# Performance work log

Measured on AMD Instinct MI355X. Metric: run time of the kernel, lower is better.

## Reference

```python
import jax, jax.numpy as jnp
from jax import lax
import numpy as np

B = 128          # batch (matches module BATCH_SIZE)
H = W = 64       # image size
E = 8            # num_experts
K = 2            # top_k
C = 1000         # num_classes (expert hidden_size)
D = 14 * 14 * 64 # flattened conv features: 64->62->31->29->14


def setup_inputs() -> dict:
    key = jax.random.key(0)
    ks = jax.random.split(key, 10)
    return {
        "x": jax.random.normal(ks[0], (B, H, W, 1), dtype=jnp.float32),
        "conv1_w": jax.random.normal(ks[1], (3, 3, 1, 32), dtype=jnp.float32) * 0.05,
        "conv1_b": jnp.zeros((32,), dtype=jnp.float32),
        "conv2_w": jax.random.normal(ks[2], (3, 3, 32, 64), dtype=jnp.float32) * 0.05,
        "conv2_b": jnp.zeros((64,), dtype=jnp.float32),
        "gate_w": jax.random.normal(ks[3], (D, E), dtype=jnp.float32) * 0.001,
        "gate_b": jnp.zeros((E,), dtype=jnp.float32),
        "expert_w": jax.random.normal(ks[4], (E, D, C), dtype=jnp.float32) * 0.001,
        "expert_b": jnp.zeros((E, C), dtype=jnp.float32),
    }


def _conv_relu(x, w, b):
    y = lax.conv_general_dilated(x, w, window_strides=(1, 1), padding="VALID",
                                 dimension_numbers=("NHWC", "HWIO", "NHWC"))
    return jax.nn.relu(y + b)


def _maxpool2(x):
    return lax.reduce_window(x, -jnp.inf, lax.max,
                             (1, 2, 2, 1), (1, 2, 2, 1), "VALID")


def reference(x, conv1_w, conv1_b, conv2_w, conv2_b, gate_w, gate_b, expert_w, expert_b):
    # conv block (dropout is identity at inference)
    h = _maxpool2(_conv_relu(x, conv1_w, conv1_b))
    h = _maxpool2(_conv_relu(h, conv2_w, conv2_b))
    h = h.reshape(h.shape[0], -1)                       # [B, D]

    # gating: softmax + top-k
    gates = jax.nn.softmax(h @ gate_w + gate_b)         # [B, E]
    topk_w, topk_i = lax.top_k(gates, K)                # [B, K]

    # all experts (tiny dense layers stacked), then gather top-k and combine
    expert_out = jnp.einsum("bd,edc->bec", h, expert_w) + expert_b  # [B, E, C]
    sel = jnp.take_along_axis(expert_out, topk_i[:, :, None], axis=1)  # [B, K, C]
    combined = jnp.sum(sel * topk_w[:, :, None], axis=1)              # [B, C]

    return jax.nn.softmax(combined)
```

## Files before the change

### kernel.cpp

```cpp
#include <hip/hip_runtime.h>
#include <math.h>

#define D_FEAT 12544
#define NC 1000
#define RB 16
#define S4 32
#define DSLICE 392
#define NIT (DSLICE/4)
#define CT2 500

__global__ __launch_bounds__(256) void k1_conv1(
    const float* __restrict__ x, const float* __restrict__ w,
    const float* __restrict__ bias, float* __restrict__ h1)
{
    int co  = threadIdx.x & 31;
    int pxi = threadIdx.x >> 5;
    int blk = blockIdx.x;
    int pxg = blk & 3;
    int py  = (blk >> 2) % 31;
    int b   = blk / (31 * 4);
    int px  = pxg * 8 + pxi;
    if (px >= 31) return;

    float wr[9];
#pragma unroll
    for (int t = 0; t < 9; ++t) wr[t] = w[t * 32 + co];
    float bb = bias[co];

    float in[4][4];
    const float* xb = x + ((size_t)(b * 64 + 2 * py) * 64 + 2 * px);
#pragma unroll
    for (int r = 0; r < 4; ++r)
#pragma unroll
        for (int c = 0; c < 4; ++c)
            in[r][c] = xb[r * 64 + c];

    float a00 = 0.f, a01 = 0.f, a10 = 0.f, a11 = 0.f;
#pragma unroll
    for (int ky = 0; ky < 3; ++ky)
#pragma unroll
        for (int kx = 0; kx < 3; ++kx) {
            float wv = wr[ky * 3 + kx];
            a00 = fmaf(in[ky][kx],     wv, a00);
            a01 = fmaf(in[ky][kx + 1], wv, a01);
            a10 = fmaf(in[ky + 1][kx], wv, a10);
            a11 = fmaf(in[ky + 1][kx + 1], wv, a11);
        }
    a00 = fmaxf(a00 + bb, 0.f);
    a01 = fmaxf(a01 + bb, 0.f);
    a10 = fmaxf(a10 + bb, 0.f);
    a11 = fmaxf(a11 + bb, 0.f);
    float v = fmaxf(fmaxf(a00, a01), fmaxf(a10, a11));
    h1[((size_t)(b * 31 + py) * 31 + px) * 32 + co] = v;
}

__global__ __launch_bounds__(448) void k2_conv2(
    const float* __restrict__ h1, const float* __restrict__ w2,
    const float* __restrict__ b2, float* __restrict__ h)
{
    __shared__ float wl[9 * 32 * 32];

    int co  = threadIdx.x & 31;
    int px  = threadIdx.x >> 5;
    int blk = blockIdx.x;
    int cob = blk & 1;
    int py  = (blk >> 1) % 14;
    int b   = blk / 28;

    for (int i = threadIdx.x; i < 9 * 32 * 32; i += 448) {
        int tapci = i >> 5;
        int col   = i & 31;
        wl[i] = w2[tapci * 64 + cob * 32 + col];
    }
    __syncthreads();

    float acc00 = 0.f, acc01 = 0.f, acc10 = 0.f, acc11 = 0.f;
    const float* base = h1 + ((size_t)(b * 31 + 2 * py) * 31 + 2 * px) * 32;

    for (int q = 0; q < 8; ++q) {
        float4 in4[4][4];
#pragma unroll
        for (int r = 0; r < 4; ++r)
#pragma unroll
            for (int c = 0; c < 4; ++c)
                in4[r][c] = *(const float4*)(base + (r * 31 + c) * 32 + q * 4);

#pragma unroll
        for (int ky = 0; ky < 3; ++ky)
#pragma unroll
            for (int kx = 0; kx < 3; ++kx) {
                int tap = ky * 3 + kx;
                const float* wp = &wl[(tap * 32 + q * 4) * 32 + co];
                float w0 = wp[0];
                float w1 = wp[32];
                float w2v = wp[64];
                float w3 = wp[96];
                acc00 = fmaf(in4[ky][kx].x, w0, acc00);
                acc00 = fmaf(in4[ky][kx].y, w1, acc00);
                acc00 = fmaf(in4[ky][kx].z, w2v, acc00);
                acc00 = fmaf(in4[ky][kx].w, w3, acc00);
                acc01 = fmaf(in4[ky][kx + 1].x, w0, acc01);
                acc01 = fmaf(in4[ky][kx + 1].y, w1, acc01);
                acc01 = fmaf(in4[ky][kx + 1].z, w2v, acc01);
                acc01 = fmaf(in4[ky][kx + 1].w, w3, acc01);
                acc10 = fmaf(in4[ky + 1][kx].x, w0, acc10);
                acc10 = fmaf(in4[ky + 1][kx].y, w1, acc10);
                acc10 = fmaf(in4[ky + 1][kx].z, w2v, acc10);
                acc10 = fmaf(in4[ky + 1][kx].w, w3, acc10);
                acc11 = fmaf(in4[ky + 1][kx + 1].x, w0, acc11);
                acc11 = fmaf(in4[ky + 1][kx + 1].y, w1, acc11);
                acc11 = fmaf(in4[ky + 1][kx + 1].z, w2v, acc11);
                acc11 = fmaf(in4[ky + 1][kx + 1].w, w3, acc11);
            }
    }

    float bb = b2[cob * 32 + co];
    acc00 = fmaxf(acc00 + bb, 0.f);
    acc01 = fmaxf(acc01 + bb, 0.f);
    acc10 = fmaxf(acc10 + bb, 0.f);
    acc11 = fmaxf(acc11 + bb, 0.f);
    float v = fmaxf(fmaxf(acc00, acc01), fmaxf(acc10, acc11));
    h[(size_t)b * D_FEAT + (py * 14 + px) * 64 + cob * 32 + co] = v;
}

__global__ __launch_bounds__(256) void k3_gate(
    const float* __restrict__ h, const float* __restrict__ gw,
    const float* __restrict__ gb, int* __restrict__ cnt,
    int* __restrict__ rowIdx, float* __restrict__ rowW,
    int* __restrict__ rowK, int* __restrict__ top2e, float* __restrict__ top2w)
{
    int b = blockIdx.x;
    int tid = threadIdx.x;
    float acc[8];
#pragma unroll
    for (int e = 0; e < 8; ++e) acc[e] = 0.f;

    const float* hb = h + (size_t)b * D_FEAT;
    for (int d = tid; d < D_FEAT; d += 256) {
        float hv = hb[d];
        float4 g0 = *(const float4*)(gw + (size_t)d * 8);
        float4 g1 = *(const float4*)(gw + (size_t)d * 8 + 4);
        acc[0] = fmaf(hv, g0.x, acc[0]);
        acc[1] = fmaf(hv, g0.y, acc[1]);
        acc[2] = fmaf(hv, g0.z, acc[2]);
        acc[3] = fmaf(hv, g0.w, acc[3]);
        acc[4] = fmaf(hv, g1.x, acc[4]);
        acc[5] = fmaf(hv, g1.y, acc[5]);
        acc[6] = fmaf(hv, g1.z, acc[6]);
        acc[7] = fmaf(hv, g1.w, acc[7]);
    }

#pragma unroll
    for (int e = 0; e < 8; ++e) {
        float v = acc[e];
        v += __shfl_down(v, 32, 64);
        v += __shfl_down(v, 16, 64);
        v += __shfl_down(v, 8, 64);
        v += __shfl_down(v, 4, 64);
        v += __shfl_down(v, 2, 64);
        v += __shfl_down(v, 1, 64);
        acc[e] = v;
    }

    __shared__ float sm[4][8];
    int wid = tid >> 6, ln = tid & 63;
    if (ln == 0) {
#pragma unroll
        for (int e = 0; e < 8; ++e) sm[wid][e] = acc[e];
    }
    __syncthreads();

    if (tid == 0) {
        float lg[8], p[8];
        float m = -1e30f;
#pragma unroll
        for (int e = 0; e < 8; ++e) {
            lg[e] = sm[0][e] + sm[1][e] + sm[2][e] + sm[3][e] + gb[e];
            m = fmaxf(m, lg[e]);
        }
        float s = 0.f;
#pragma unroll
        for (int e = 0; e < 8; ++e) { p[e] = expf(lg[e] - m); s += p[e]; }
        float inv = 1.f / s;
#pragma unroll
        for (int e = 0; e < 8; ++e) p[e] *= inv;

        int i0 = 0;
#pragma unroll
        for (int e = 1; e < 8; ++e) if (p[e] > p[i0]) i0 = e;
        int i1 = (i0 == 0) ? 1 : 0;
#pragma unroll
        for (int e = 0; e < 8; ++e) if (e != i0 && p[e] > p[i1]) i1 = e;

        int pos0 = atomicAdd(&cnt[i0], 1);
        rowIdx[i0 * 128 + pos0] = b;
        rowW[i0 * 128 + pos0] = p[i0];
        rowK[i0 * 128 + pos0] = 0;
        int pos1 = atomicAdd(&cnt[i1], 1);
        rowIdx[i1 * 128 + pos1] = b;
        rowW[i1 * 128 + pos1] = p[i1];
        rowK[i1 * 128 + pos1] = 1;

        top2e[b * 2]     = i0;
        top2e[b * 2 + 1] = i1;
        top2w[b * 2]     = p[i0];
        top2w[b * 2 + 1] = p[i1];
    }
}

#define FMA_ROW2(A, HV, W0, W1, W2, W3)                         \
    do {                                                        \
        (A).x = fmaf((HV).x, (W0).x, (A).x);                    \
        (A).x = fmaf((HV).y, (W1).x, (A).x);                    \
        (A).x = fmaf((HV).z, (W2).x, (A).x);                    \
        (A).x = fmaf((HV).w, (W3).x, (A).x);                    \
        (A).y = fmaf((HV).x, (W0).y, (A).y);                    \
        (A).y = fmaf((HV).y, (W1).y, (A).y);                    \
        (A).y = fmaf((HV).z, (W2).y, (A).y);                    \
        (A).y = fmaf((HV).w, (W3).y, (A).y);                    \
    } while (0)

__global__ __launch_bounds__(256) void k4_expert(
    const float* __restrict__ h, const float* __restrict__ ew,
    const int* __restrict__ cnt, const int* __restrict__ rowIdx,
    const float* __restrict__ rowW, const int* __restrict__ rowK,
    float* __restrict__ part)
{
    __shared__ float h_lds[RB * DSLICE];
    __shared__ int   roff_s[RB];

    int tid = threadIdx.x;
    int bid = blockIdx.x;
    int s  = bid & 31;
    int ct = (bid >> 5) & 1;
    int e  = (bid >> 6) & 7;
    int rc = bid >> 9;

    int n = cnt[e];
    int rbase = rc * RB;
    if (rbase >= n) return;
    int nrows = n - rbase; if (nrows > RB) nrows = RB;

    if (tid < RB) {
        roff_s[tid] = (tid < nrows) ? rowIdx[e * 128 + rbase + tid] * D_FEAT : -1;
    }
    __syncthreads();

    int dbase = s * DSLICE;
    for (int i = tid; i < RB * (DSLICE / 4); i += 256) {
        int r = i / (DSLICE / 4);
        int q = i - r * (DSLICE / 4);
        int ro = roff_s[r];
        float4 v = make_float4(0.f, 0.f, 0.f, 0.f);
        if (ro >= 0) v = *(const float4*)(h + ro + dbase + q * 4);
        *(float4*)&h_lds[r * DSLICE + q * 4] = v;
    }
    __syncthreads();

    if (tid < 250) {
        const float* wp = ew + ((size_t)e * D_FEAT + dbase) * NC + ct * CT2 + tid * 2;
        bool g1 = (nrows > 8);

        float2 acc[RB];
#pragma unroll
        for (int r = 0; r < RB; ++r) acc[r] = make_float2(0.f, 0.f);

        float2 wA0 = *(const float2*)(wp);
        float2 wA1 = *(const float2*)(wp + (size_t)NC);
        float2 wA2 = *(const float2*)(wp + (size_t)2 * NC);
        float2 wA3 = *(const float2*)(wp + (size_t)3 * NC);

        for (int it = 0; it < NIT; ++it) {
            const float* np = wp + (size_t)4 * NC;
            float2 wB0, wB1, wB2, wB3;
            if (it < NIT - 1) {
                wB0 = *(const float2*)(np);
                wB1 = *(const float2*)(np + (size_t)NC);
                wB2 = *(const float2*)(np + (size_t)2 * NC);
                wB3 = *(const float2*)(np + (size_t)3 * NC);
            }
            int d = it * 4;
            const float* hp = &h_lds[d];
#pragma unroll
            for (int r = 0; r < 8; ++r) {
                float4 hv = *(const float4*)(hp + r * DSLICE);
                FMA_ROW2(acc[r], hv, wA0, wA1, wA2, wA3);
            }
            if (g1) {
#pragma unroll
                for (int r = 8; r < 16; ++r) {
                    float4 hv = *(const float4*)(hp + r * DSLICE);
                    FMA_ROW2(acc[r], hv, wA0, wA1, wA2, wA3);
                }
            }
            wp = np;
            wA0 = wB0; wA1 = wB1; wA2 = wB2; wA3 = wB3;
        }

        int cc = ct * CT2 + tid * 2;
#pragma unroll
        for (int r = 0; r < RB; ++r) {
            if (r < nrows) {
                int pos = e * 128 + rbase + r;
                float wgt = rowW[pos];
                int ri = rowIdx[pos];
                int kk = rowK[pos];
                float2 o = make_float2(wgt * acc[r].x, wgt * acc[r].y);
                *(float2*)&part[(((size_t)s * 128 + ri) * 2 + kk) * NC + cc] = o;
            }
        }
    }
}

__global__ __launch_bounds__(256) void k5_softmax(
    const float* __restrict__ part, const float* __restrict__ eb,
    const int* __restrict__ top2e, const float* __restrict__ top2w,
    float* __restrict__ out)
{
    int b = blockIdx.x;
    int tid = threadIdx.x;
    __shared__ float red[4];

    int e0 = top2e[b * 2], e1 = top2e[b * 2 + 1];
    float tw0 = top2w[b * 2], tw1 = top2w[b * 2 + 1];

    bool act = (tid < 250);
    int c0 = tid * 4;
    float4 v = make_float4(-1e30f, -1e30f, -1e30f, -1e30f);
    if (act) {
        float4 a = make_float4(0.f, 0.f, 0.f, 0.f);
        for (int s = 0; s < S4; ++s) {
            const float* p0 = part + (((size_t)s * 128 + b) * 2) * NC + c0;
            float4 q0 = *(const float4*)p0;
            float4 q1 = *(const float4*)(p0 + NC);
            a.x += q0.x + q1.x;
            a.y += q0.y + q1.y;
            a.z += q0.z + q1.z;
            a.w += q0.w + q1.w;
        }
        float4 b0 = *(const float4*)(eb + e0 * NC + c0);
        float4 b1 = *(const float4*)(eb + e1 * NC + c0);
        v.x = a.x + tw0 * b0.x + tw1 * b1.x;
        v.y = a.y + tw0 * b0.y + tw1 * b1.y;
        v.z = a.z + tw0 * b0.z + tw1 * b1.z;
        v.w = a.w + tw0 * b0.w + tw1 * b1.w;
    }

    float m = fmaxf(fmaxf(v.x, v.y), fmaxf(v.z, v.w));
#pragma unroll
    for (int off = 32; off >= 1; off >>= 1)
        m = fmaxf(m, __shfl_xor(m, off, 64));
    int wid = tid >> 6, ln = tid & 63;
    if (ln == 0) red[wid] = m;
    __syncthreads();
    m = fmaxf(fmaxf(red[0], red[1]), fmaxf(red[2], red[3]));
    __syncthreads();

    float ex, ey, ez, ew2;
    ex = act ? expf(v.x - m) : 0.f;
    ey = act ? expf(v.y - m) : 0.f;
    ez = act ? expf(v.z - m) : 0.f;
    ew2 = act ? expf(v.w - m) : 0.f;
    float ssum = ex + ey + ez + ew2;
#pragma unroll
    for (int off = 32; off >= 1; off >>= 1)
        ssum += __shfl_xor(ssum, off, 64);
    if (ln == 0) red[wid] = ssum;
    __syncthreads();
    ssum = red[0] + red[1] + red[2] + red[3];
    float inv = 1.f / ssum;

    if (act) {
        float4 o = make_float4(ex * inv, ey * inv, ez * inv, ew2 * inv);
        *(float4*)&out[(size_t)b * NC + c0] = o;
    }
}

extern "C" void kernel_launch(void* const* d_in, const int* in_sizes, int n_in,
                              void* d_out, int out_size, void* d_ws, size_t ws_size,
                              hipStream_t stream) {
    const float* x   = (const float*)d_in[0];
    const float* c1w = (const float*)d_in[1];
    const float* c1b = (const float*)d_in[2];
    const float* c2w = (const float*)d_in[3];
    const float* c2b = (const float*)d_in[4];
    const float* gw  = (const float*)d_in[5];
    const float* gb  = (const float*)d_in[6];
    const float* ew  = (const float*)d_in[7];
    const float* eb  = (const float*)d_in[8];
    float* out = (float*)d_out;

    char* ws = (char*)d_ws;
    int*   cnt    = (int*)  (ws + 0);
    int*   rowIdx = (int*)  (ws + 64);
    float* rowW   = (float*)(ws + 4160);
    int*   rowK   = (int*)  (ws + 8256);
    int*   top2e  = (int*)  (ws + 12352);
    float* top2w  = (float*)(ws + 13376);
    float* h      = (float*)(ws + 16384);
    float* h1     = (float*)(ws + 6438912);
    float* part   = (float*)(ws + 6438912);

    hipMemsetAsync(cnt, 0, 32, stream);

    k1_conv1<<<128 * 31 * 4, 256, 0, stream>>>(x, c1w, c1b, h1);
    k2_conv2<<<128 * 14 * 2, 448, 0, stream>>>(h1, c2w, c2b, h);
    k3_gate<<<128, 256, 0, stream>>>(h, gw, gb, cnt, rowIdx, rowW, rowK, top2e, top2w);
    k4_expert<<<S4 * 2 * 8 * 8, 256, 0, stream>>>(h, ew, cnt, rowIdx, rowW, rowK, part);
    k5_softmax<<<128, 256, 0, stream>>>(part, eb, top2e, top2w, out);
}
```

Baseline: 300.3 us.

## Retile expert GEMM to 40-row blocks over all columns and drop memset

The expert kernel now processes up to 40 routed rows per block, covering all 1000 output columns with 512 threads, and splits D into 64 slices of 196 instead of 32 slices of 392. Each expert weight element is reused across more batch rows, so fewer weight re-reads are needed when an expert gets more than 16 rows. The separate memset of the expert counters is folded into the first conv kernel. In exchange, each thread keeps 40 float2 accumulators, which raises register pressure, and rows beyond nrows do wasted FMAs on zeros. The final softmax also has to reduce twice as many partial slices.

```diff
diff --git a/kernel.cpp b/kernel.cpp
--- a/kernel.cpp
+++ b/kernel.cpp
@@ -3,16 +3,18 @@
 
 #define D_FEAT 12544
 #define NC 1000
-#define RB 16
-#define S4 32
-#define DSLICE 392
-#define NIT (DSLICE/4)
-#define CT2 500
+#define RMAX 40
+#define S64 64
+#define DSL 196
+#define NIT4 (DSL/4)
 
 __global__ __launch_bounds__(256) void k1_conv1(
     const float* __restrict__ x, const float* __restrict__ w,
-    const float* __restrict__ bias, float* __restrict__ h1)
+    const float* __restrict__ bias, float* __restrict__ h1,
+    int* __restrict__ cnt)
 {
+    if (blockIdx.x == 0 && threadIdx.x < 8) cnt[threadIdx.x] = 0;
+
     int co  = threadIdx.x & 31;
     int pxi = threadIdx.x >> 5;
     int blk = blockIdx.x;
@@ -220,93 +222,83 @@
         (A).y = fmaf((HV).w, (W3).y, (A).y);                    \
     } while (0)
 
-__global__ __launch_bounds__(256) void k4_expert(
+__global__ __launch_bounds__(512, 4) void k4_expert(
     const float* __restrict__ h, const float* __restrict__ ew,
     const int* __restrict__ cnt, const int* __restrict__ rowIdx,
     const float* __restrict__ rowW, const int* __restrict__ rowK,
     float* __restrict__ part)
 {
-    __shared__ float h_lds[RB * DSLICE];
-    __shared__ int   roff_s[RB];
-
-    int tid = threadIdx.x;
-    int bid = blockIdx.x;
-    int s  = bid & 31;
-    int ct = (bid >> 5) & 1;
-    int e  = (bid >> 6) & 7;
-    int rc = bid >> 9;
+    __shared__ float h_lds[RMAX * DSL];
+    __shared__ int   roff_s[RMAX];
+
+    int tid  = threadIdx.x;
+    int bid  = blockIdx.x;
+    int rc   = bid >> 9;
+    int base = bid & 511;
+    int s    = base & 63;
+    int e    = base >> 6;
 
     int n = cnt[e];
-    int rbase = rc * RB;
+    int rbase = rc * RMAX;
     if (rbase >= n) return;
-    int nrows = n - rbase; if (nrows > RB) nrows = RB;
-
-    if (tid < RB) {
+    int nrows = n - rbase; if (nrows > RMAX) nrows = RMAX;
+
+    if (tid < RMAX) {
         roff_s[tid] = (tid < nrows) ? rowIdx[e * 128 + rbase + tid] * D_FEAT : -1;
     }
     __syncthreads();
 
-    int dbase = s * DSLICE;
-    for (int i = tid; i < RB * (DSLICE / 4); i += 256) {
-        int r = i / (DSLICE / 4);
-        int q = i - r * (DSLICE / 4);
+    int dbase = s * DSL;
+    for (int i = tid; i < RMAX * NIT4; i += 512) {
+        int r = i / NIT4;
+        int q = i - r * NIT4;
         int ro = roff_s[r];
         float4 v = make_float4(0.f, 0.f, 0.f, 0.f);
         if (ro >= 0) v = *(const float4*)(h + ro + dbase + q * 4);
-        *(float4*)&h_lds[r * DSLICE + q * 4] = v;
-    }
-    __syncthreads();
-
-    if (tid < 250) {
-        const float* wp = ew + ((size_t)e * D_FEAT + dbase) * NC + ct * CT2 + tid * 2;
-        bool g1 = (nrows > 8);
-
-        float2 acc[RB];
-#pragma unroll
-        for (int r = 0; r < RB; ++r) acc[r] = make_float2(0.f, 0.f);
+        *(float4*)&h_lds[r * DSL + q * 4] = v;
+    }
+    __syncthreads();
+
+    if (tid < 500) {
+        const float* wp = ew + ((size_t)e * D_FEAT + dbase) * NC + tid * 2;
+
+        float2 acc[RMAX];
+#pragma unroll
+        for (int r = 0; r < RMAX; ++r) acc[r] = make_float2(0.f, 0.f);
 
         float2 wA0 = *(const float2*)(wp);
         float2 wA1 = *(const float2*)(wp + (size_t)NC);
         float2 wA2 = *(const float2*)(wp + (size_t)2 * NC);
         float2 wA3 = *(const float2*)(wp + (size_t)3 * NC);
 
-        for (int it = 0; it < NIT; ++it) {
+        for (int it = 0; it < NIT4; ++it) {
             const float* np = wp + (size_t)4 * NC;
             float2 wB0, wB1, wB2, wB3;
-            if (it < NIT - 1) {
+            if (it < NIT4 - 1) {
                 wB0 = *(const float2*)(np);
                 wB1 = *(const float2*)(np + (size_t)NC);
                 wB2 = *(const float2*)(np + (size_t)2 * NC);
                 wB3 = *(const float2*)(np + (size_t)3 * NC);
             }
-            int d = it * 4;
-            const float* hp = &h_lds[d];
-#pragma unroll
-            for (int r = 0; r < 8; ++r) {
-                float4 hv = *(const float4*)(hp + r * DSLICE);
+            const float* hp = &h_lds[it * 4];
+#pragma unroll
+            for (int r = 0; r < RMAX; ++r) {
+                float4 hv = *(const float4*)(hp + r * DSL);
                 FMA_ROW2(acc[r], hv, wA0, wA1, wA2, wA3);
-            }
-            if (g1) {
-#pragma unroll
-                for (int r = 8; r < 16; ++r) {
-                    float4 hv = *(const float4*)(hp + r * DSLICE);
-                    FMA_ROW2(acc[r], hv, wA0, wA1, wA2, wA3);
-                }
             }
             wp = np;
             wA0 = wB0; wA1 = wB1; wA2 = wB2; wA3 = wB3;
         }
 
-        int cc = ct * CT2 + tid * 2;
-#pragma unroll
-        for (int r = 0; r < RB; ++r) {
+#pragma unroll
+        for (int r = 0; r < RMAX; ++r) {
             if (r < nrows) {
                 int pos = e * 128 + rbase + r;
                 float wgt = rowW[pos];
                 int ri = rowIdx[pos];
                 int kk = rowK[pos];
                 float2 o = make_float2(wgt * acc[r].x, wgt * acc[r].y);
-                *(float2*)&part[(((size_t)s * 128 + ri) * 2 + kk) * NC + cc] = o;
+                *(float2*)&part[(((size_t)s * 128 + ri) * 2 + kk) * NC + tid * 2] = o;
             }
         }
     }
@@ -329,7 +321,7 @@
     float4 v = make_float4(-1e30f, -1e30f, -1e30f, -1e30f);
     if (act) {
         float4 a = make_float4(0.f, 0.f, 0.f, 0.f);
-        for (int s = 0; s < S4; ++s) {
+        for (int s = 0; s < S64; ++s) {
             const float* p0 = part + (((size_t)s * 128 + b) * 2) * NC + c0;
             float4 q0 = *(const float4*)p0;
             float4 q1 = *(const float4*)(p0 + NC);
@@ -401,11 +393,9 @@
     float* h1     = (float*)(ws + 6438912);
     float* part   = (float*)(ws + 6438912);
 
-    hipMemsetAsync(cnt, 0, 32, stream);
-
-    k1_conv1<<<128 * 31 * 4, 256, 0, stream>>>(x, c1w, c1b, h1);
+    k1_conv1<<<128 * 31 * 4, 256, 0, stream>>>(x, c1w, c1b, h1, cnt);
     k2_conv2<<<128 * 14 * 2, 448, 0, stream>>>(h1, c2w, c2b, h);
     k3_gate<<<128, 256, 0, stream>>>(h, gw, gb, cnt, rowIdx, rowW, rowK, top2e, top2w);
-    k4_expert<<<S4 * 2 * 8 * 8, 256, 0, stream>>>(h, ew, cnt, rowIdx, rowW, rowK, part);
+    k4_expert<<<4 * 8 * 64, 512, 0, stream>>>(h, ew, cnt, rowIdx, rowW, rowK, part);
     k5_softmax<<<128, 256, 0, stream>>>(part, eb, top2e, top2w, out);
 }
```

After: 405.5 us. 1.35x slower.
